# Optimization experiments

Hardware: AMD Instinct MI355X
Metric: run time of the kernel (lower is better)

Reference implementation:

```python
import jax, jax.numpy as jnp
import numpy as np
from jax import lax

B, N, M = 16, 4096, 1024
RADII = [0.1, 0.2]
KS = [32, 64]
MLP_SPECS = [[64, 64, 128], [64, 96, 128]]
C_IN = 64 + 3  # use_xyz
EPS = 1e-5


def setup_inputs() -> dict:
    key = jax.random.key(0)
    ks = jax.random.split(key, 32)
    inp = {
        "pc": jax.random.uniform(ks[0], (B, 3, N), jnp.float32),
        "features": jax.random.normal(ks[1], (B, 64, N), jnp.float32),
    }
    ki = 2
    for i, spec in enumerate(MLP_SPECS):
        cin = C_IN
        for j, cout in enumerate(spec):
            inp[f"W{i}{j}"] = jax.random.normal(ks[ki], (cout, cin), jnp.float32) * (1.0 / np.sqrt(cin)); ki += 1
            inp[f"b{i}{j}"] = jnp.zeros((cout,), jnp.float32)
            inp[f"g{i}{j}"] = jnp.ones((cout,), jnp.float32)
            inp[f"be{i}{j}"] = jnp.zeros((cout,), jnp.float32)
            cin = cout
    return inp


def farthest_point_sampling(pc_t, m):
    # pc_t: [B, N, 3] -> [B, m] int32 indices. Sequential FPS via scan.
    b, n, _ = pc_t.shape
    init = (jnp.full((b, n), 1e10, pc_t.dtype), jnp.zeros((b,), jnp.int32))
    def step(carry, _):
        dmin, far = carry
        centroid = jnp.take_along_axis(pc_t, far[:, None, None], axis=1)  # [B,1,3]
        dist = jnp.sum((pc_t - centroid) ** 2, axis=-1)                    # [B,N]
        dmin = jnp.minimum(dmin, dist)
        nxt = jnp.argmax(dmin, axis=-1).astype(jnp.int32)
        return (dmin, nxt), far
    _, idxs = lax.scan(step, init, None, length=m)
    return idxs.T  # [B, m]


def ball_query(pc_t, centers_t, r, k):
    # pc_t: [B,N,3], centers_t: [B,M,3] -> [B,M,k] int32.
    # Original CUDA semantics: first k points (in index order) within radius;
    # pad with the first found index if fewer than k.
    n = pc_t.shape[1]
    d2 = jnp.sum((centers_t[:, :, None, :] - pc_t[:, None, :, :]) ** 2, axis=-1)  # [B,M,N]
    cand = jnp.where(d2 < r * r, jnp.arange(n, dtype=jnp.int32), jnp.int32(n))
    neg, _ = lax.top_k(-cand, k)   # k smallest candidate indices
    idx = -neg
    first = idx[:, :, :1]
    return jnp.where(idx == n, first, idx)


def group_points(feat, idx):
    # feat: [B,C,N], idx: [B,M,K] -> [B,C,M,K]
    return jax.vmap(lambda f, i: f[:, i])(feat, idx)


def _mlp_bn_relu(x, params):
    # x: [B,C,M,K]; 1x1 conv == channel matmul, BN over (B,M,K) (training stats), ReLU
    for (W, b, g, be) in params:
        x = jnp.einsum('oc,bcmk->bomk', W, x) + b[None, :, None, None]
        mu = jnp.mean(x, axis=(0, 2, 3), keepdims=True)
        var = jnp.var(x, axis=(0, 2, 3), keepdims=True)
        x = (x - mu) * lax.rsqrt(var + EPS) * g[None, :, None, None] + be[None, :, None, None]
        x = jax.nn.relu(x)
    return x


def _forward(pc, features, params):
    pc_t = pc.transpose(0, 2, 1)                       # [B,N,3]
    samp = farthest_point_sampling(pc_t, M)            # [B,M]
    new_pc = jnp.take_along_axis(pc, jnp.broadcast_to(samp[:, None, :], (B, 3, M)), axis=2)  # [B,3,M]
    new_pc_t = new_pc.transpose(0, 2, 1)               # [B,M,3]
    outs = []
    for i in range(len(RADII)):
        gidx = ball_query(pc_t, new_pc_t, RADII[i], KS[i])          # [B,M,K]
        xyz = group_points(pc, gidx) - new_pc[:, :, :, None]        # [B,3,M,K]
        grp = group_points(features, gidx)                          # [B,64,M,K]
        x = jnp.concatenate([xyz, grp], axis=1)                     # [B,67,M,K]
        x = _mlp_bn_relu(x, params[i])
        outs.append(jnp.max(x, axis=-1))                            # [B,Cout,M]
    return new_pc, jnp.concatenate(outs, axis=1)


def reference(pc, features,
              W00, b00, g00, be00, W01, b01, g01, be01, W02, b02, g02, be02,
              W10, b10, g10, be10, W11, b11, g11, be11, W12, b12, g12, be12):
    params = [
        [(W00, b00, g00, be00), (W01, b01, g01, be01), (W02, b02, g02, be02)],
        [(W10, b10, g10, be10), (W11, b11, g11, be11), (W12, b12, g12, be12)],
    ]
    return _forward(pc, features, params)
```

## Files before the change

kernel.cpp:

```cpp
#include <hip/hip_runtime.h>
#include <cstdio>
#include <cstdint>


constexpr int BATCH = 16, NPTS = 4096, MCTR = 1024;
constexpr int BM = BATCH * MCTR;
constexpr int NSLOT = 32;

typedef short bf16x8 __attribute__((ext_vector_type(8)));
typedef float f32x4  __attribute__((ext_vector_type(4)));
typedef float f32x2  __attribute__((ext_vector_type(2)));

__device__ __forceinline__ ushort f2bf(float f) {
  uint32_t u = __float_as_uint(f);
  u += 0x7fffu + ((u >> 16) & 1u);
  return (ushort)(u >> 16);
}
__device__ __forceinline__ uint32_t packbf(float a, float b) {
  return (uint32_t)f2bf(a) | ((uint32_t)f2bf(b) << 16);
}
__device__ __forceinline__ unsigned long long umax64(unsigned long long a,
                                                     unsigned long long b) {
  return (a > b) ? a : b;
}

template <int CTRL>
__device__ __forceinline__ unsigned long long dpp_max(unsigned long long k) {
  int lo = (int)(uint32_t)k, hi = (int)(uint32_t)(k >> 32);
  uint32_t plo = (uint32_t)__builtin_amdgcn_update_dpp(0, lo, CTRL, 0xf, 0xf, false);
  uint32_t phi = (uint32_t)__builtin_amdgcn_update_dpp(0, hi, CTRL, 0xf, 0xf, false);
  unsigned long long pk = ((unsigned long long)phi << 32) | plo;
  return (pk > k) ? pk : k;
}

__device__ __forceinline__ void fps_body(int b, int t, const float* __restrict__ pc,
                                         float* __restrict__ newpc_out,
                                         char* __restrict__ smem) {
  float* lX = (float*)smem;
  float* lY = lX + NPTS;
  float* lZ = lY + NPTS;
  int*   sampL = (int*)(smem + 3 * NPTS * 4);
  unsigned long long* wkey =
      (unsigned long long*)(smem + 3 * NPTS * 4 + MCTR * 4);
  const int lane = t & 63;
  const int w = t >> 6;
  const float* px = pc + (size_t)b * 3 * NPTS;
  f32x2 X2[8], Y2[8], Z2[8], D2[8];
#pragma unroll
  for (int j = 0; j < 16; j++) {
    int p = t + 256 * j;
    float x = px[p], y = px[NPTS + p], z = px[2 * NPTS + p];
    X2[j >> 1][j & 1] = x; Y2[j >> 1][j & 1] = y; Z2[j >> 1][j & 1] = z;
    D2[j >> 1][j & 1] = 1e10f;
    lX[p] = x; lY[p] = y; lZ[p] = z;
  }
  if (t == 0) sampL[0] = 0;
  __syncthreads();
  int far = 0;
  for (int it = 1; it < MCTR; it++) {
    float cx = lX[far], cy = lY[far], cz = lZ[far];
    float bv = -1.0f; int bi = 0;
    {
#pragma clang fp contract(off)
      f32x2 cx2 = {cx, cx}, cy2 = {cy, cy}, cz2 = {cz, cz};
#pragma unroll
      for (int j2 = 0; j2 < 8; j2++) {
        f32x2 dx = X2[j2] - cx2, dy = Y2[j2] - cy2, dz = Z2[j2] - cz2;
        f32x2 d = dx * dx + dy * dy + dz * dz;
        f32x2 dm;
        dm[0] = fminf(D2[j2][0], d[0]);
        dm[1] = fminf(D2[j2][1], d[1]);
        D2[j2] = dm;
        bool g0 = dm[0] > bv;
        bv = g0 ? dm[0] : bv; bi = g0 ? t + 256 * (2 * j2) : bi;
        bool g1 = dm[1] > bv;
        bv = g1 ? dm[1] : bv; bi = g1 ? t + 256 * (2 * j2 + 1) : bi;
      }
    }
    unsigned long long key =
        ((unsigned long long)__float_as_uint(bv) << 32) | (unsigned)(~bi);
    key = dpp_max<0xB1>(key);
    key = dpp_max<0x4E>(key);
    key = dpp_max<0x124>(key);
    key = dpp_max<0x128>(key);
    key = dpp_max<0x142>(key);
    key = dpp_max<0x143>(key);
    if (lane == 63) wkey[(it & 1) * 4 + w] = key;
    __syncthreads();
    const ulonglong2* kp = (const ulonglong2*)(wkey + (it & 1) * 4);
    ulonglong2 k0 = kp[0], k1 = kp[1];
    unsigned long long kk = umax64(umax64(k0.x, k0.y), umax64(k1.x, k1.y));
    far = (int)(~(unsigned)kk);
    if (t == 0) sampL[it] = far;
  }
  __syncthreads();
  float* npc = newpc_out + (size_t)b * 3 * MCTR;
  for (int m = t; m < MCTR; m += 256) {
    int f = sampL[m];
    npc[m] = lX[f]; npc[MCTR + m] = lY[f]; npc[2 * MCTR + m] = lZ[f];
  }
}

__device__ __forceinline__ void u_body(const float* __restrict__ feat,
                                       const float* __restrict__ W,
                                       const float* __restrict__ bias,
                                       ushort* __restrict__ Ub, int ub,
                                       char* __restrict__ smem) {
  float* wl = (float*)smem;
  int t = threadIdx.x;
#pragma unroll
  for (int i = 0; i < 16; i++) {
    int r = t + 256 * i;
    wl[r] = W[(r & 63) * 67 + 3 + (r >> 6)];
  }
  __syncthreads();
  int gid = ub * 256 + t;
  int b = gid >> 12, n = gid & 4095;
  float acc[64];
#pragma unroll
  for (int o = 0; o < 64; o++) acc[o] = bias[o];
  const float* fb = feat + (size_t)b * 64 * NPTS + n;
  for (int c = 0; c < 64; c++) {
    float x = fb[(size_t)c * NPTS];
    const f32x4* w4 = (const f32x4*)(wl + c * 64);
#pragma unroll
    for (int q = 0; q < 16; q++) {
      f32x4 wv = w4[q];
      acc[4 * q + 0] = fmaf(wv[0], x, acc[4 * q + 0]);
      acc[4 * q + 1] = fmaf(wv[1], x, acc[4 * q + 1]);
      acc[4 * q + 2] = fmaf(wv[2], x, acc[4 * q + 2]);
      acc[4 * q + 3] = fmaf(wv[3], x, acc[4 * q + 3]);
    }
  }
  uint4* o4 = (uint4*)(Ub + (size_t)gid * 64);
#pragma unroll
  for (int qq = 0; qq < 8; qq++)
    o4[qq] = make_uint4(packbf(acc[8*qq+0], acc[8*qq+1]), packbf(acc[8*qq+2], acc[8*qq+3]),
                        packbf(acc[8*qq+4], acc[8*qq+5]), packbf(acc[8*qq+6], acc[8*qq+7]));
}

__global__ __launch_bounds__(256) void fused_stageA(
    const float* __restrict__ pc, const float* __restrict__ feat,
    const float* __restrict__ W00, const float* __restrict__ b00,
    const float* __restrict__ W01, const float* __restrict__ W02,
    const float* __restrict__ W10, const float* __restrict__ b10,
    const float* __restrict__ W11, const float* __restrict__ W12,
    float* __restrict__ newpc_out, ushort* __restrict__ Ub0,
    ushort* __restrict__ Ub1, float* __restrict__ wt, ushort* __restrict__ wf) {
  __shared__ __align__(16) char smem[3 * NPTS * 4 + MCTR * 4 + 64];
  int bx = blockIdx.x, t = threadIdx.x;
  if (bx < 16) { fps_body(bx, t, pc, newpc_out, smem); return; }
  if (bx < 528) {
    int ub = bx - 16;
    if (ub < 256) u_body(feat, W00, b00, Ub0, ub, smem);
    else          u_body(feat, W10, b10, Ub1, ub - 256, smem);
    return;
  }
  int e = (bx - 528) * 256 + t;
  if (e < 4096) { wt[e] = W00[(e & 63) * 67 + 3 + (e >> 6)]; return; }
  if (e < 4288) { int r = e - 4096; wt[e] = W00[(r & 63) * 67 + (r >> 6)]; return; }
  if (e < 8384) { int r = e - 4288; wt[e] = W10[(r & 63) * 67 + 3 + (r >> 6)]; return; }
  if (e < 8576) { int r = e - 8384; wt[e] = W10[(r & 63) * 67 + (r >> 6)]; return; }
  int e2 = e - 8576;
  if (e2 >= 30720) return;
  const float* W; int CIN, MT, off;
  if (e2 < 4096)       { W = W01; CIN = 64; MT = 4; off = 0; }
  else if (e2 < 12288) { W = W02; CIN = 64; MT = 8; off = 4096; }
  else if (e2 < 18432) { W = W11; CIN = 64; MT = 6; off = 12288; }
  else                 { W = W12; CIN = 96; MT = 8; off = 18432; }
  int r = e2 - off;
  int j = r & 7, lane = (r >> 3) & 63, fm = r >> 9;
  int kc = fm / MT, mt = fm % MT;
  int out_ch = mt * 16 + (lane & 15);
  int in_ch  = kc * 32 + (lane >> 4) * 8 + j;
  wf[e2] = f2bf(W[out_ch * CIN + in_ch]);
}

template <int K>
__device__ __forceinline__ void ballq_body(int bx, const float* __restrict__ pc,
                                           const float* __restrict__ newpc,
                                           int* __restrict__ gidx, float r2) {
  int lane = threadIdx.x & 63;
  int wave = threadIdx.x >> 6;
  int center = bx * 4 + wave;
  int b = center >> 10, m = center & 1023;
  const float* nb = newpc + (size_t)b * 3 * MCTR + m;
  float cx = nb[0], cy = nb[MCTR], cz = nb[2 * MCTR];
  const float* px = pc + (size_t)b * 3 * NPTS;
  int cnt = 0;
  int firstn = 0x7fffffff;
  for (int chunk = 0; chunk < NPTS / 64 && cnt < K; chunk++) {
    int n = chunk * 64 + lane;
    float dx = __fsub_rn(cx, px[n]);
    float dy = __fsub_rn(cy, px[NPTS + n]);
    float dz = __fsub_rn(cz, px[2 * NPTS + n]);
    float d2 = __fadd_rn(__fadd_rn(__fmul_rn(dx, dx), __fmul_rn(dy, dy)), __fmul_rn(dz, dz));
    bool in = d2 < r2;
    unsigned long long ball = __ballot(in);
    int pos = cnt + (int)__popcll(ball & ((1ull << lane) - 1ull));
    if (in && pos < K) gidx[(size_t)center * K + pos] = n;
    if (in && pos == 0) firstn = n;
    cnt += (int)__popcll(ball);
  }
#pragma unroll
  for (int off = 32; off; off >>= 1) firstn = min(firstn, __shfl_xor(firstn, off));
  if (lane < K && lane >= cnt) gidx[(size_t)center * K + lane] = firstn;
}

__global__ __launch_bounds__(256) void ballq_fused(const float* __restrict__ pc,
                                                   const float* __restrict__ newpc,
                                                   int* __restrict__ gidx0,
                                                   int* __restrict__ gidx1,
                                                   float r2a, float r2b) {
  int bx = blockIdx.x;
  if (bx < BM / 4) ballq_body<32>(bx, pc, newpc, gidx0, r2a);
  else             ballq_body<64>(bx - BM / 4, pc, newpc, gidx1, r2b);
}

__device__ __forceinline__ void layer1_compute(const ushort* __restrict__ Ub,
                                               const float* __restrict__ pc,
                                               const float* __restrict__ newpc,
                                               const float* __restrict__ Wt1,
                                               int b, int m, int idx, float* v1) {
  float dx = pc[((size_t)b * 3 + 0) * NPTS + idx] - newpc[((size_t)b * 3 + 0) * MCTR + m];
  float dy = pc[((size_t)b * 3 + 1) * NPTS + idx] - newpc[((size_t)b * 3 + 1) * MCTR + m];
  float dz = pc[((size_t)b * 3 + 2) * NPTS + idx] - newpc[((size_t)b * 3 + 2) * MCTR + m];
  const uint4* u4 = (const uint4*)(Ub + (size_t)((b << 12) + idx) * 64);
#pragma unroll
  for (int qq = 0; qq < 8; qq++) {
    uint4 u = u4[qq];
    v1[8*qq+0] = __uint_as_float(u.x << 16);
    v1[8*qq+1] = __uint_as_float(u.x & 0xffff0000u);
    v1[8*qq+2] = __uint_as_float(u.y << 16);
    v1[8*qq+3] = __uint_as_float(u.y & 0xffff0000u);
    v1[8*qq+4] = __uint_as_float(u.z << 16);
    v1[8*qq+5] = __uint_as_float(u.z & 0xffff0000u);
    v1[8*qq+6] = __uint_as_float(u.w << 16);
    v1[8*qq+7] = __uint_as_float(u.w & 0xffff0000u);
  }
#pragma unroll
  for (int o = 0; o < 64; o++) v1[o] = fmaf(Wt1[o], dx, v1[o]);
#pragma unroll
  for (int o = 0; o < 64; o++) v1[o] = fmaf(Wt1[64 + o], dy, v1[o]);
#pragma unroll
  for (int o = 0; o < 64; o++) v1[o] = fmaf(Wt1[128 + o], dz, v1[o]);
}

__device__ __forceinline__ void wave_reduce32(const float* vals, float* tile, int t,
                                              float* swrow, int co) {
  float* myrow = tile + t * 32;
  int rsw = t & 31;
#pragma unroll
  for (int o = 0; o < 32; o++) myrow[o ^ rsw] = vals[o];
  __syncthreads();
  int lane = t & 63;
  int ch = lane & 31, sub = lane >> 5;
  const float* base = tile + (t & ~63) * 32;
  float s = 0.f, s2 = 0.f;
#pragma unroll
  for (int r = 0; r < 32; r++) {
    int row = sub * 32 + r;
    float v = base[row * 32 + (ch ^ (row & 31))];
    s += v; s2 = fmaf(v, v, s2);
  }
  float st = s + __shfl_xor(s, 32);
  float st2 = s2 + __shfl_xor(s2, 32);
  if (sub == 0) {
    swrow[co + ch] += st;
    swrow[128 + co + ch] += st2;
  }
  __syncthreads();
}

template <int K>
__device__ __forceinline__ void l1_body(
    int bx, const ushort* __restrict__ Ub, const float* __restrict__ pc,
    const float* __restrict__ newpc, const int* __restrict__ gidx,
    const float* __restrict__ Wt1, float* __restrict__ stats,
    float* tile, float* sAcc ) {
  const int t = threadIdx.x;
  const int w = t >> 6;
  const int p = bx * 128 + t;
  const int bm = p / K;
  const int b = bm >> 10, m = bm & 1023;
  const int idx = gidx[p];
  for (int i = t; i < 512; i += 128) sAcc[i] = 0.f;

  float v1[64];
  layer1_compute(Ub, pc, newpc, Wt1, b, m, idx, v1);

  wave_reduce32(v1,      tile, t, sAcc + w * 256, 0);
  wave_reduce32(v1 + 32, tile, t, sAcc + w * 256, 32);

  __syncthreads();
  float* dst = stats + (size_t)(bx & (NSLOT - 1)) * 128;
  for (int i = t; i < 64; i += 128) {
    atomicAdd(&dst[i],      sAcc[i]       + sAcc[256 + i]);
    atomicAdd(&dst[64 + i], sAcc[128 + i] + sAcc[256 + 128 + i]);
  }
}

__global__ __launch_bounds__(128, 2) void l1_fused(
    const ushort* __restrict__ Ub0, const ushort* __restrict__ Ub1,
    const float* __restrict__ pc, const float* __restrict__ newpc,
    const int* __restrict__ gidx0, const int* __restrict__ gidx1,
    const float* __restrict__ Wt1a, const float* __restrict__ Wt1b,
    float* __restrict__ st0, float* __restrict__ st1) {
  __shared__ float tile[128 * 32];
  __shared__ float sAccW[2][256];
  constexpr int NB0 = (BM * 32) / 128;
  int bx = blockIdx.x;
  if (bx < NB0) l1_body<32>(bx, Ub0, pc, newpc, gidx0, Wt1a, st0, tile, &sAccW[0][0]);
  else          l1_body<64>(bx - NB0, Ub1, pc, newpc, gidx1, Wt1b, st1, tile, &sAccW[0][0]);
}

template <int K, int C2, int NL>
__global__ __launch_bounds__(256, 2) void mfma_pass(
    const ushort* __restrict__ Ub, const float* __restrict__ pc,
    const float* __restrict__ newpc, const int* __restrict__ gidx,
    const float* __restrict__ Wt1,
    const ushort* __restrict__ W2f, const ushort* __restrict__ W3f,
    const float* __restrict__ b2, const float* __restrict__ b3,
    const float* __restrict__ st1, const float* __restrict__ g1,
    const float* __restrict__ be1,
    const float* __restrict__ st2, const float* __restrict__ g2,
    const float* __restrict__ be2, float invP,
    float* __restrict__ stats, ushort* __restrict__ maxbuf,
    ushort* __restrict__ minbuf) {
  constexpr int MT2 = C2 / 16, KC3 = C2 / 32;
  constexpr int CLs = (NL == 2) ? C2 : 128;
  constexpr int SSTR = CLs + 4;
  __shared__ __align__(16) ushort x1f[4][2][4][64][8];
  __shared__ __align__(16) ushort x2f[(NL == 3) ? 4 : 1][KC3][4][16][8];
  __shared__ __align__(16) ushort x3s[4][16][SSTR];
  __shared__ float sAccW[4][256];
  __shared__ __align__(16) float cA1s[64], cC1s[64];
  __shared__ __align__(16) float cA2s[(NL == 3) ? C2 : 4], cC2s[(NL == 3) ? C2 : 4];

  const int t = threadIdx.x, w = t >> 6, lane = t & 63;
  const int q = lane >> 4, n = lane & 15;
  const int p = blockIdx.x * 256 + t;
  const int bm = p / K;
  const int b = bm >> 10, m = bm & 1023;
  const int idx = gidx[p];

  if (t < 64) {
    float s = 0.f, s2 = 0.f;
    for (int sl = 0; sl < NSLOT; sl++) {
      s  += st1[sl * 128 + t];
      s2 += st1[sl * 128 + 64 + t];
    }
    float mu = s * invP;
    float var = fmaf(s2, invP, -(mu * mu));
    float a = g1[t] / sqrtf(var + 1e-5f);
    cA1s[t] = a;
    cC1s[t] = fmaf(-a, mu, be1[t]);
  }
  if (NL == 3 && t >= 128 && t < 128 + C2) {
    int c = t - 128;
    float s = 0.f, s2 = 0.f;
    for (int sl = 0; sl < NSLOT; sl++) {
      s  += st2[sl * 2 * C2 + c];
      s2 += st2[sl * 2 * C2 + C2 + c];
    }
    float mu = s * invP;
    float var = fmaf(s2, invP, -(mu * mu));
    float a = g2[c] / sqrtf(var + 1e-5f);
    cA2s[c] = a;
    cC2s[c] = fmaf(-a, mu, be2[c]);
  }
  __syncthreads();

  {
    float v1[64];
    layer1_compute(Ub, pc, newpc, Wt1, b, m, idx, v1);
    int nw = t & 63;
#pragma unroll
    for (int g = 0; g < 8; g++) {
      uint32_t d0, d1, d2, d3;
      int c = g * 8;
      d0 = packbf(fmaxf(0.f, fmaf(cA1s[c+0], v1[c+0], cC1s[c+0])),
                  fmaxf(0.f, fmaf(cA1s[c+1], v1[c+1], cC1s[c+1])));
      d1 = packbf(fmaxf(0.f, fmaf(cA1s[c+2], v1[c+2], cC1s[c+2])),
                  fmaxf(0.f, fmaf(cA1s[c+3], v1[c+3], cC1s[c+3])));
      d2 = packbf(fmaxf(0.f, fmaf(cA1s[c+4], v1[c+4], cC1s[c+4])),
                  fmaxf(0.f, fmaf(cA1s[c+5], v1[c+5], cC1s[c+5])));
      d3 = packbf(fmaxf(0.f, fmaf(cA1s[c+6], v1[c+6], cC1s[c+6])),
                  fmaxf(0.f, fmaf(cA1s[c+7], v1[c+7], cC1s[c+7])));
      *(uint4*)&x1f[w][g >> 2][g & 3][nw][0] = make_uint4(d0, d1, d2, d3);
    }
  }
  asm volatile("s_waitcnt lgkmcnt(0)" ::: "memory");

  bf16x8 A2[2 * MT2];
#pragma unroll
  for (int i = 0; i < 2 * MT2; i++) A2[i] = *(const bf16x8*)(W2f + (i * 64 + lane) * 8);
  bf16x8 A3[(NL == 3) ? KC3 * 8 : 1];
  if (NL == 3) {
#pragma unroll
    for (int i = 0; i < KC3 * 8; i++) A3[i] = *(const bf16x8*)(W3f + (i * 64 + lane) * 8);
  }

  float sS0 = 0.f, sS1 = 0.f, sS20 = 0.f, sS21 = 0.f;
  float mx0 = -3.4e38f, mx1 = -3.4e38f, mn0 = 3.4e38f, mn1 = 3.4e38f;

#pragma unroll
  for (int tl = 0; tl < 4; tl++) {
    bf16x8 bf2[2];
#pragma unroll
    for (int kc = 0; kc < 2; kc++)
      bf2[kc] = *(const bf16x8*)&x1f[w][kc][q][tl * 16 + n][0];
    f32x4 acc2[MT2];
#pragma unroll
    for (int mt = 0; mt < MT2; mt++) acc2[mt] = *(const f32x4*)(b2 + mt * 16 + q * 4);
#pragma unroll
    for (int kc = 0; kc < 2; kc++)
#pragma unroll
      for (int mt = 0; mt < MT2; mt++)
        acc2[mt] = __builtin_amdgcn_mfma_f32_16x16x32_bf16(A2[kc * MT2 + mt], bf2[kc],
                                                           acc2[mt], 0, 0, 0);
    if (NL == 2) {
#pragma unroll
      for (int mt = 0; mt < MT2; mt++) {
        int ch0 = mt * 16 + q * 4;
        *(uint2*)&x3s[w][n][ch0] = make_uint2(packbf(acc2[mt][0], acc2[mt][1]),
                                              packbf(acc2[mt][2], acc2[mt][3]));
      }
    } else {
#pragma unroll
      for (int mt = 0; mt < MT2; mt++) {
        int ch0 = mt * 16 + q * 4;
        f32x4 ca = *(const f32x4*)(cA2s + ch0);
        f32x4 cc = *(const f32x4*)(cC2s + ch0);
        float r0 = fmaxf(0.f, fmaf(ca[0], acc2[mt][0], cc[0]));
        float r1 = fmaxf(0.f, fmaf(ca[1], acc2[mt][1], cc[1]));
        float r2 = fmaxf(0.f, fmaf(ca[2], acc2[mt][2], cc[2]));
        float r3 = fmaxf(0.f, fmaf(ca[3], acc2[mt][3], cc[3]));
        int kc2 = ch0 >> 5, q2 = (ch0 >> 3) & 3, j0 = ch0 & 7;
        *(uint2*)&x2f[w][kc2][q2][n][j0] = make_uint2(packbf(r0, r1), packbf(r2, r3));
      }
      asm volatile("s_waitcnt lgkmcnt(0)" ::: "memory");
      f32x4 acc3[8];
#pragma unroll
      for (int mt = 0; mt < 8; mt++) acc3[mt] = *(const f32x4*)(b3 + mt * 16 + q * 4);
#pragma unroll
      for (int kc = 0; kc < KC3; kc++) {
        bf16x8 bf3 = *(const bf16x8*)&x2f[w][kc][q][n][0];
#pragma unroll
        for (int mt = 0; mt < 8; mt++)
          acc3[mt] = __builtin_amdgcn_mfma_f32_16x16x32_bf16(A3[kc * 8 + mt], bf3,
                                                             acc3[mt], 0, 0, 0);
      }
#pragma unroll
      for (int mt = 0; mt < 8; mt++) {
        int ch0 = mt * 16 + q * 4;
        *(uint2*)&x3s[w][n][ch0] = make_uint2(packbf(acc3[mt][0], acc3[mt][1]),
                                              packbf(acc3[mt][2], acc3[mt][3]));
      }
    }
    asm volatile("s_waitcnt lgkmcnt(0)" ::: "memory");
    if (2 * lane < CLs) {
#pragma unroll
      for (int pos = 0; pos < 16; pos++) {
        uint32_t u = *(const uint32_t*)&x3s[w][pos][2 * lane];
        float v0 = __uint_as_float(u << 16);
        float v1v = __uint_as_float(u & 0xffff0000u);
        sS0 += v0;  sS20 = fmaf(v0, v0, sS20);
        sS1 += v1v; sS21 = fmaf(v1v, v1v, sS21);
        if (NL == 3) {
          mx0 = fmaxf(mx0, v0);  mn0 = fminf(mn0, v0);
          mx1 = fmaxf(mx1, v1v); mn1 = fminf(mn1, v1v);
        }
      }
    }
    if (NL == 3) {
      bool fl = (K == 64) ? (tl == 3) : ((tl & 1) == 1);
      if (fl) {
        int center = (K == 64) ? (blockIdx.x * 4 + w)
                               : (blockIdx.x * 8 + w * 2 + (tl >> 1));
        *(uint32_t*)&maxbuf[(size_t)center * 128 + 2 * lane] = packbf(mx0, mx1);
        *(uint32_t*)&minbuf[(size_t)center * 128 + 2 * lane] = packbf(mn0, mn1);
        mx0 = mx1 = -3.4e38f; mn0 = mn1 = 3.4e38f;
      }
    }
    asm volatile("s_waitcnt lgkmcnt(0)" ::: "memory");
  }

  {
    int ch = 2 * lane;
    if (ch < CLs) {
      sAccW[w][ch] = sS0;        sAccW[w][ch + 1] = sS1;
      sAccW[w][CLs + ch] = sS20; sAccW[w][CLs + ch + 1] = sS21;
    }
  }
  __syncthreads();
  float* dst = stats + (size_t)(blockIdx.x & (NSLOT - 1)) * (2 * CLs);
  for (int i = t; i < 2 * CLs; i += 256)
    atomicAdd(&dst[i], sAccW[0][i] + sAccW[1][i] + sAccW[2][i] + sAccW[3][i]);
}

__global__ __launch_bounds__(256) void outwrite_fused(
    const ushort* __restrict__ mx0buf, const ushort* __restrict__ mn0buf,
    const ushort* __restrict__ mx1buf, const ushort* __restrict__ mn1buf,
    const float* __restrict__ st30, const float* __restrict__ g30,
    const float* __restrict__ be30, float invP0,
    const float* __restrict__ st31, const float* __restrict__ g31,
    const float* __restrict__ be31, float invP1,
    float* __restrict__ out_feat) {
  __shared__ float tile[64 * 130];
  __shared__ float cA3s[128], cC3s[128];
  int bx = blockIdx.x;
  const ushort* mxb; const ushort* mnb;
  const float* st; const float* g; const float* be; float invP;
  int chOff, c0;
  if (bx < BM / 64) {
    mxb = mx0buf; mnb = mn0buf; st = st30; g = g30; be = be30; invP = invP0;
    chOff = 0; c0 = bx * 64;
  } else {
    mxb = mx1buf; mnb = mn1buf; st = st31; g = g31; be = be31; invP = invP1;
    chOff = 128; c0 = (bx - BM / 64) * 64;
  }
  int t = threadIdx.x;
  if (t < 128) {
    float s = 0.f, s2 = 0.f;
    for (int sl = 0; sl < NSLOT; sl++) {
      s  += st[sl * 256 + t];
      s2 += st[sl * 256 + 128 + t];
    }
    float mu = s * invP;
    float var = fmaf(s2, invP, -(mu * mu));
    float a = g[t] / sqrtf(var + 1e-5f);
    cA3s[t] = a;
    cC3s[t] = fmaf(-a, mu, be[t]);
  }
  __syncthreads();
#pragma unroll
  for (int i = 0; i < 32; i++) {
    int e = i * 256 + t;
    int lc = e >> 7, o = e & 127;
    float a = cA3s[o];
    float mv = __uint_as_float(((uint32_t)mxb[(size_t)(c0 + lc) * 128 + o]) << 16);
    float nv = __uint_as_float(((uint32_t)mnb[(size_t)(c0 + lc) * 128 + o]) << 16);
    float v = (a >= 0.f) ? fmaf(a, mv, cC3s[o]) : fmaf(a, nv, cC3s[o]);
    tile[lc * 130 + o] = fmaxf(v, 0.f);
  }
  __syncthreads();
  int b = c0 >> 10, m0 = c0 & 1023;
#pragma unroll
  for (int j = 0; j < 32; j++) {
    int e = j * 256 + t;
    int lm = e & 63, o = e >> 6;
    out_feat[((size_t)(b * 256 + chOff + o)) * MCTR + m0 + lm] = tile[lm * 130 + o];
  }
}

extern "C" void kernel_launch(void* const* d_in, const int* in_sizes, int n_in,
                              void* d_out, int out_size, void* d_ws, size_t ws_size,
                              hipStream_t stream) {
  (void)in_sizes; (void)n_in; (void)out_size;
  const float* pc   = (const float*)d_in[0];
  const float* feat = (const float*)d_in[1];
  const float *Wp[2][3], *bp[2][3], *gp[2][3], *bep[2][3];
  for (int s = 0; s < 2; s++)
    for (int l = 0; l < 3; l++) {
      int base = 2 + (s * 3 + l) * 4;
      Wp[s][l]  = (const float*)d_in[base + 0];
      bp[s][l]  = (const float*)d_in[base + 1];
      gp[s][l]  = (const float*)d_in[base + 2];
      bep[s][l] = (const float*)d_in[base + 3];
    }

  char* ws = (char*)d_ws;
  float*  statsR  = (float*) (ws + 0x10000);
  float*  wt      = (float*) (ws + 0x42000);
  ushort* wf      = (ushort*)(ws + 0x50000);
  ushort* Ub0     = (ushort*)(ws + 0x100000);
  ushort* Ub1     = (ushort*)(ws + 0x900000);
  int*    gidx0   = (int*)   (ws + 0x1100000);
  int*    gidx1   = (int*)   (ws + 0x1300000);
  ushort* mxb0    = (ushort*)(ws + 0x1700000);
  ushort* mnb0    = (ushort*)(ws + 0x1B00000);
  ushort* mxb1    = (ushort*)(ws + 0x1F00000);
  ushort* mnb1    = (ushort*)(ws + 0x2300000);
  const unsigned long long WS_NEEDED = 0x2700000ULL;
  if (ws_size < WS_NEEDED) {
    fprintf(stderr, "[kernel] ws too small: %zu < %llu\n", ws_size, WS_NEEDED);
    return;
  }

  float* out_newpc = (float*)d_out;
  float* out_feat  = (float*)d_out + (size_t)BATCH * 3 * MCTR;

  const int P0 = BM * 32, P1 = BM * 64;
  const int LSTRIDE = NSLOT * 256;
  float* st10 = statsR + 0 * LSTRIDE, *st20 = statsR + 1 * LSTRIDE, *st30 = statsR + 2 * LSTRIDE;
  float* st11 = statsR + 3 * LSTRIDE, *st21 = statsR + 4 * LSTRIDE, *st31 = statsR + 5 * LSTRIDE;

  hipMemsetAsync(statsR, 0, 6 * NSLOT * 256 * sizeof(float), stream);
  fused_stageA<<<682, 256, 0, stream>>>(pc, feat,
                                        Wp[0][0], bp[0][0], Wp[0][1], Wp[0][2],
                                        Wp[1][0], bp[1][0], Wp[1][1], Wp[1][2],
                                        out_newpc, Ub0, Ub1, wt, wf);
  ballq_fused<<<BM / 2, 256, 0, stream>>>(pc, out_newpc, gidx0, gidx1,
                                          (float)(0.1 * 0.1), (float)(0.2 * 0.2));

  l1_fused<<<P0 / 128 + P1 / 128, 128, 0, stream>>>(Ub0, Ub1, pc, out_newpc,
                                                    gidx0, gidx1,
                                                    wt + 4096, wt + 8384, st10, st11);

  mfma_pass<32, 64, 2><<<P0 / 256, 256, 0, stream>>>(Ub0, pc, out_newpc, gidx0,
      wt + 4096, wf + 0, wf + 4096, bp[0][1], bp[0][2],
      st10, gp[0][0], bep[0][0], nullptr, nullptr, nullptr, 1.0f / P0,
      st20, nullptr, nullptr);
  mfma_pass<64, 96, 2><<<P1 / 256, 256, 0, stream>>>(Ub1, pc, out_newpc, gidx1,
      wt + 8384, wf + 12288, wf + 18432, bp[1][1], bp[1][2],
      st11, gp[1][0], bep[1][0], nullptr, nullptr, nullptr, 1.0f / P1,
      st21, nullptr, nullptr);

  mfma_pass<32, 64, 3><<<P0 / 256, 256, 0, stream>>>(Ub0, pc, out_newpc, gidx0,
      wt + 4096, wf + 0, wf + 4096, bp[0][1], bp[0][2],
      st10, gp[0][0], bep[0][0], st20, gp[0][1], bep[0][1], 1.0f / P0,
      st30, mxb0, mnb0);
  mfma_pass<64, 96, 3><<<P1 / 256, 256, 0, stream>>>(Ub1, pc, out_newpc, gidx1,
      wt + 8384, wf + 12288, wf + 18432, bp[1][1], bp[1][2],
      st11, gp[1][0], bep[1][0], st21, gp[1][1], bep[1][1], 1.0f / P1,
      st31, mxb1, mnb1);

  outwrite_fused<<<2 * (BM / 64), 256, 0, stream>>>(mxb0, mnb0, mxb1, mnb1,
                                                    st30, gp[0][2], bep[0][2], 1.0f / P0,
                                                    st31, gp[1][2], bep[1][2], 1.0f / P1,
                                                    out_feat);
}
```

Baseline: 1.126 ms.

## Fuse ball query into layer-1 stats kernel via shared-memory neighbor indices

Merges the ball-query kernel and the layer-1 BN statistics kernel into one launch. Each 256-thread block finds neighbors for 256/K centers, writes them both to global memory for later passes and to shared memory, then runs layer-1 on those indices without re-reading gidx from global. Block size for the layer-1 part grows from 128 to 256 threads, which doubles shared tile usage and may lower occupancy. The sequential ball-query scan now runs several centers per wave before the compute phase.

```diff
diff --git a/kernel.cpp b/kernel.cpp
--- a/kernel.cpp
+++ b/kernel.cpp
@@ -176,47 +176,6 @@
   wf[e2] = f2bf(W[out_ch * CIN + in_ch]);
 }
 
-template <int K>
-__device__ __forceinline__ void ballq_body(int bx, const float* __restrict__ pc,
-                                           const float* __restrict__ newpc,
-                                           int* __restrict__ gidx, float r2) {
-  int lane = threadIdx.x & 63;
-  int wave = threadIdx.x >> 6;
-  int center = bx * 4 + wave;
-  int b = center >> 10, m = center & 1023;
-  const float* nb = newpc + (size_t)b * 3 * MCTR + m;
-  float cx = nb[0], cy = nb[MCTR], cz = nb[2 * MCTR];
-  const float* px = pc + (size_t)b * 3 * NPTS;
-  int cnt = 0;
-  int firstn = 0x7fffffff;
-  for (int chunk = 0; chunk < NPTS / 64 && cnt < K; chunk++) {
-    int n = chunk * 64 + lane;
-    float dx = __fsub_rn(cx, px[n]);
-    float dy = __fsub_rn(cy, px[NPTS + n]);
-    float dz = __fsub_rn(cz, px[2 * NPTS + n]);
-    float d2 = __fadd_rn(__fadd_rn(__fmul_rn(dx, dx), __fmul_rn(dy, dy)), __fmul_rn(dz, dz));
-    bool in = d2 < r2;
-    unsigned long long ball = __ballot(in);
-    int pos = cnt + (int)__popcll(ball & ((1ull << lane) - 1ull));
-    if (in && pos < K) gidx[(size_t)center * K + pos] = n;
-    if (in && pos == 0) firstn = n;
-    cnt += (int)__popcll(ball);
-  }
-#pragma unroll
-  for (int off = 32; off; off >>= 1) firstn = min(firstn, __shfl_xor(firstn, off));
-  if (lane < K && lane >= cnt) gidx[(size_t)center * K + lane] = firstn;
-}
-
-__global__ __launch_bounds__(256) void ballq_fused(const float* __restrict__ pc,
-                                                   const float* __restrict__ newpc,
-                                                   int* __restrict__ gidx0,
-                                                   int* __restrict__ gidx1,
-                                                   float r2a, float r2b) {
-  int bx = blockIdx.x;
-  if (bx < BM / 4) ballq_body<32>(bx, pc, newpc, gidx0, r2a);
-  else             ballq_body<64>(bx - BM / 4, pc, newpc, gidx1, r2b);
-}
-
 __device__ __forceinline__ void layer1_compute(const ushort* __restrict__ Ub,
                                                const float* __restrict__ pc,
                                                const float* __restrict__ newpc,
@@ -273,18 +232,54 @@
 }
 
 template <int K>
-__device__ __forceinline__ void l1_body(
-    int bx, const ushort* __restrict__ Ub, const float* __restrict__ pc,
-    const float* __restrict__ newpc, const int* __restrict__ gidx,
+__device__ __forceinline__ void ballq_l1_body(
+    int bx, const float* __restrict__ pc, const float* __restrict__ newpc,
+    int* __restrict__ gidx, float r2, const ushort* __restrict__ Ub,
     const float* __restrict__ Wt1, float* __restrict__ stats,
-    float* tile, float* sAcc ) {
+    int* lgidx, float* tile, float* sAcc ) {
   const int t = threadIdx.x;
-  const int w = t >> 6;
-  const int p = bx * 128 + t;
+  const int lane = t & 63, w = t >> 6;
+  for (int i = t; i < 1024; i += 256) sAcc[i] = 0.f;
+  constexpr int CPB = 256 / K;
+  constexpr int CPW = CPB / 4;
+#pragma unroll
+  for (int cc = 0; cc < CPW; cc++) {
+    int lc = w * CPW + cc;
+    int center = bx * CPB + lc;
+    int b = center >> 10, m = center & 1023;
+    const float* nb = newpc + (size_t)b * 3 * MCTR + m;
+    float cx = nb[0], cy = nb[MCTR], cz = nb[2 * MCTR];
+    const float* px = pc + (size_t)b * 3 * NPTS;
+    int cnt = 0;
+    int firstn = 0x7fffffff;
+    for (int chunk = 0; chunk < NPTS / 64 && cnt < K; chunk++) {
+      int n = chunk * 64 + lane;
+      float dx = __fsub_rn(cx, px[n]);
+      float dy = __fsub_rn(cy, px[NPTS + n]);
+      float dz = __fsub_rn(cz, px[2 * NPTS + n]);
+      float d2 = __fadd_rn(__fadd_rn(__fmul_rn(dx, dx), __fmul_rn(dy, dy)), __fmul_rn(dz, dz));
+      bool in = d2 < r2;
+      unsigned long long ball = __ballot(in);
+      int pos = cnt + (int)__popcll(ball & ((1ull << lane) - 1ull));
+      if (in && pos < K) {
+        gidx[(size_t)center * K + pos] = n;
+        lgidx[lc * K + pos] = n;
+      }
+      if (in && pos == 0) firstn = n;
+      cnt += (int)__popcll(ball);
+    }
+#pragma unroll
+    for (int off = 32; off; off >>= 1) firstn = min(firstn, __shfl_xor(firstn, off));
+    if (lane < K && lane >= cnt) {
+      gidx[(size_t)center * K + lane] = firstn;
+      lgidx[lc * K + lane] = firstn;
+    }
+  }
+  __syncthreads();
+  const int p = bx * 256 + t;
   const int bm = p / K;
   const int b = bm >> 10, m = bm & 1023;
-  const int idx = gidx[p];
-  for (int i = t; i < 512; i += 128) sAcc[i] = 0.f;
+  const int idx = lgidx[t];
 
   float v1[64];
   layer1_compute(Ub, pc, newpc, Wt1, b, m, idx, v1);
@@ -294,24 +289,32 @@
 
   __syncthreads();
   float* dst = stats + (size_t)(bx & (NSLOT - 1)) * 128;
-  for (int i = t; i < 64; i += 128) {
-    atomicAdd(&dst[i],      sAcc[i]       + sAcc[256 + i]);
-    atomicAdd(&dst[64 + i], sAcc[128 + i] + sAcc[256 + 128 + i]);
-  }
-}
-
-__global__ __launch_bounds__(128, 2) void l1_fused(
+  for (int i = t; i < 64; i += 256) {
+    atomicAdd(&dst[i],      sAcc[i]       + sAcc[256 + i] + sAcc[512 + i] + sAcc[768 + i]);
+    atomicAdd(&dst[64 + i], sAcc[128 + i] + sAcc[256 + 128 + i] +
+                            sAcc[512 + 128 + i] + sAcc[768 + 128 + i]);
+  }
+}
+
+constexpr int NBL0 = BM / 8;
+constexpr int NBL1 = BM / 4;
+
+__global__ __launch_bounds__(256) void ballq_l1_fused(
+    const float* __restrict__ pc, const float* __restrict__ newpc,
+    int* __restrict__ gidx0, int* __restrict__ gidx1, float r2a, float r2b,
     const ushort* __restrict__ Ub0, const ushort* __restrict__ Ub1,
-    const float* __restrict__ pc, const float* __restrict__ newpc,
-    const int* __restrict__ gidx0, const int* __restrict__ gidx1,
     const float* __restrict__ Wt1a, const float* __restrict__ Wt1b,
     float* __restrict__ st0, float* __restrict__ st1) {
-  __shared__ float tile[128 * 32];
-  __shared__ float sAccW[2][256];
-  constexpr int NB0 = (BM * 32) / 128;
+  __shared__ float tile[256 * 32];
+  __shared__ float sAccW[4][256];
+  __shared__ int lgidx[256];
   int bx = blockIdx.x;
-  if (bx < NB0) l1_body<32>(bx, Ub0, pc, newpc, gidx0, Wt1a, st0, tile, &sAccW[0][0]);
-  else          l1_body<64>(bx - NB0, Ub1, pc, newpc, gidx1, Wt1b, st1, tile, &sAccW[0][0]);
+  if (bx < NBL0)
+    ballq_l1_body<32>(bx, pc, newpc, gidx0, r2a, Ub0, Wt1a, st0,
+                      lgidx, tile, &sAccW[0][0]);
+  else
+    ballq_l1_body<64>(bx - NBL0, pc, newpc, gidx1, r2b, Ub1, Wt1b, st1,
+                      lgidx, tile, &sAccW[0][0]);
 }
 
 template <int K, int C2, int NL>
@@ -601,12 +604,12 @@
                                         Wp[0][0], bp[0][0], Wp[0][1], Wp[0][2],
                                         Wp[1][0], bp[1][0], Wp[1][1], Wp[1][2],
                                         out_newpc, Ub0, Ub1, wt, wf);
-  ballq_fused<<<BM / 2, 256, 0, stream>>>(pc, out_newpc, gidx0, gidx1,
-                                          (float)(0.1 * 0.1), (float)(0.2 * 0.2));
-
-  l1_fused<<<P0 / 128 + P1 / 128, 128, 0, stream>>>(Ub0, Ub1, pc, out_newpc,
-                                                    gidx0, gidx1,
-                                                    wt + 4096, wt + 8384, st10, st11);
+
+  ballq_l1_fused<<<NBL0 + NBL1, 256, 0, stream>>>(pc, out_newpc,
+                                                  gidx0, gidx1,
+                                                  (float)(0.1 * 0.1), (float)(0.2 * 0.2),
+                                                  Ub0, Ub1, wt + 4096, wt + 8384,
+                                                  st10, st11);
 
   mfma_pass<32, 64, 2><<<P0 / 256, 256, 0, stream>>>(Ub0, pc, out_newpc, gidx0,
       wt + 4096, wf + 0, wf + 4096, bp[0][1], bp[0][2],
```

Result: slower. 1.198 ms (+6.4%).
